# Kernel optimization log

Hardware: AMD Instinct MI355X
Metric: run time of the kernel (lower is better)

## Reference

```python
import jax, jax.numpy as jnp
import numpy as np
from jax import lax


def _farthest_point_sample(xyz, npoint):
    """Iterative FPS, faithful to the torch loop. xyz: [B,N,3] -> centroids [B,npoint] int32."""
    B, N, _ = xyz.shape
    barycenter = jnp.mean(xyz, axis=1, keepdims=True)            # [B,1,3]
    d0 = jnp.sum((xyz - barycenter) ** 2, axis=-1)               # [B,N]
    farthest = jnp.argmax(d0, axis=1)                            # [B]
    distance = jnp.full((B, N), 1e10, dtype=xyz.dtype)
    selected = jnp.zeros((B, N), dtype=bool)
    batch_idx = jnp.arange(B)

    def step(carry, _):
        distance, selected, farthest = carry
        selected = selected.at[batch_idx, farthest].set(True)
        centroid = jnp.take_along_axis(xyz, farthest[:, None, None], axis=1)  # [B,1,3]
        d = jnp.sum((xyz - centroid) ** 2, axis=-1)              # [B,N]
        d = jnp.where(selected, 0.0, d)                          # torch: dist[selected_mask]=0
        distance = jnp.minimum(distance, d)                      # torch: distance[mask]=dist[mask]
        nxt = jnp.argmax(distance, axis=-1)
        return (distance, selected, nxt), farthest

    _, cents = lax.scan(step, (distance, selected, farthest), None, length=npoint)
    return jnp.transpose(cents)                                   # [B, npoint]


def _assign_points_to_clusters(xyz, centroids):
    """Assign every point to nearest centroid. Vectorized over batch (no python loop)."""
    cpts = jnp.take_along_axis(xyz, centroids[:, :, None], axis=1)          # [B,P,3]
    # [B,N,P] pairwise squared distances
    dist = jnp.sum((xyz[:, :, None, :] - cpts[:, None, :, :]) ** 2, axis=-1)
    return jnp.argmin(dist, axis=-1)                                         # [B,N]


def setup_inputs() -> dict:
    key = jax.random.key(0)
    B, N = 8, 100000
    xyz = jax.random.normal(key, (B, N, 3), dtype=jnp.float32)
    return {"xyz": xyz, "npoint": 64}


def reference(xyz, npoint):
    centroids = _farthest_point_sample(xyz, npoint)               # [B,P] int
    clusters = _assign_points_to_clusters(xyz, centroids)         # [B,N] int
    centroid_xyz = jnp.take_along_axis(xyz, centroids[:, :, None], axis=1)  # [B,P,3] float
    return centroid_xyz, centroids, clusters
```

## Files before the change

### kernel.cpp

```cpp
#include <hip/hip_runtime.h>

#define BATCHES 8
#define NPTS    100000
#define NPOINT  64
#define BPB     16
#define NTHREADS 512
#define WPB     (NTHREADS / 64)
#define TPB     (BPB * NTHREADS)
#define KMAX    13
#define TAILN   (NPTS - (KMAX - 1) * TPB)

#define WS_BARY_OFF 0
#define WS_CNT_OFF  3072
#define WS_SLOT_OFF 4096
#define WS_CTRL_BYTES (WS_SLOT_OFF + BATCHES * NPOINT * BPB * 8)

__device__ __forceinline__ float sq3(float dx, float dy, float dz) {
    return __fadd_rn(__fadd_rn(__fmul_rn(dx, dx), __fmul_rn(dy, dy)), __fmul_rn(dz, dz));
}

__global__ __launch_bounds__(NTHREADS, 4)
void fps_kernel(const float* __restrict__ xyz, float* __restrict__ out,
                unsigned char* __restrict__ ws)
{
    double* baryPart = (double*)(ws + WS_BARY_OFF);
    unsigned int* cnt = (unsigned int*)(ws + WS_CNT_OFF);
    unsigned long long* slots = (unsigned long long*)(ws + WS_SLOT_OFF);

    const int b    = blockIdx.x & 7;
    const int blk  = blockIdx.x >> 3;
    const int tid  = threadIdx.x;
    const int wid  = tid >> 6;
    const int lane = tid & 63;
    const int t    = blk * NTHREADS + tid;

    const float* xb = xyz + (size_t)b * NPTS * 3;

    __shared__ double bred[WPB][3];
    __shared__ unsigned long long kred[WPB];
    __shared__ float s_c[3];
    __shared__ int s_far;

    float px[KMAX], py[KMAX], pz[KMAX], dist[KMAX];
    float bestd[KMAX]; int besti[KMAX];
    const int nk = (t < TAILN) ? KMAX : (KMAX - 1);

    double sx = 0.0, sy = 0.0, sz = 0.0;
    #pragma unroll
    for (int k = 0; k < KMAX; k++) {
        if (k < nk) {
            int p = t + k * TPB;
            float x = xb[p * 3 + 0], y = xb[p * 3 + 1], z = xb[p * 3 + 2];
            px[k] = x; py[k] = y; pz[k] = z; dist[k] = 1e10f;
            bestd[k] = 3.4e38f; besti[k] = 0;
            sx += (double)x; sy += (double)y; sz += (double)z;
        }
    }
    for (int off = 32; off > 0; off >>= 1) {
        sx += __shfl_down(sx, off); sy += __shfl_down(sy, off); sz += __shfl_down(sz, off);
    }
    if (lane == 0) { bred[wid][0] = sx; bred[wid][1] = sy; bred[wid][2] = sz; }
    __syncthreads();
    if (tid == 0) {
        double ax = 0, ay = 0, az = 0;
        for (int w = 0; w < WPB; w++) { ax += bred[w][0]; ay += bred[w][1]; az += bred[w][2]; }
        double* dst = baryPart + ((size_t)b * BPB + blk) * 3;
        dst[0] = ax; dst[1] = ay; dst[2] = az;
        __hip_atomic_fetch_add(&cnt[b], 1u, __ATOMIC_ACQ_REL, __HIP_MEMORY_SCOPE_AGENT);
        while (__hip_atomic_load(&cnt[b], __ATOMIC_ACQUIRE, __HIP_MEMORY_SCOPE_AGENT) < BPB)
            __builtin_amdgcn_s_sleep(2);
        double mx = 0, my = 0, mz = 0;
        for (int q = 0; q < BPB; q++) {
            const double* s2 = baryPart + ((size_t)b * BPB + q) * 3;
            mx += s2[0]; my += s2[1]; mz += s2[2];
        }
        s_c[0] = (float)(mx / (double)NPTS);
        s_c[1] = (float)(my / (double)NPTS);
        s_c[2] = (float)(mz / (double)NPTS);
    }
    __syncthreads();
    const float bx = s_c[0], by = s_c[1], bz = s_c[2];

    float bd = -1.0f; int bp = 0;
    #pragma unroll
    for (int k = 0; k < KMAX; k++) {
        if (k < nk) {
            int p = t + k * TPB;
            float d = sq3(__fsub_rn(px[k], bx), __fsub_rn(py[k], by), __fsub_rn(pz[k], bz));
            if (d > bd) { bd = d; bp = p; }
        }
    }
    unsigned long long key = (((unsigned long long)__float_as_uint(bd)) << 32)
                             | (unsigned)(0xFFFFFFFFu - (unsigned)bp);

    for (int e = 0; e < NPOINT; e++) {
        unsigned long long wmax = key;
        for (int m = 32; m > 0; m >>= 1) {
            unsigned long long o = __shfl_xor(wmax, m); if (o > wmax) wmax = o;
        }
        if (lane == 0) kred[wid] = wmax;
        __syncthreads();

        if (wid == 0) {
            unsigned long long v = (lane < WPB) ? kred[lane] : 0ull;
            for (int m = 4; m > 0; m >>= 1) {
                unsigned long long o = __shfl_xor(v, m, 8); if (o > v) v = o;
            }
            unsigned long long* row = &slots[((size_t)b * NPOINT + e) * BPB];
            if (lane == 0)
                __hip_atomic_store(&row[blk], v, __ATOMIC_RELAXED, __HIP_MEMORY_SCOPE_AGENT);
            unsigned long long w = 0;
            if (lane < BPB) {
                while ((w = __hip_atomic_load(&row[lane], __ATOMIC_RELAXED,
                                              __HIP_MEMORY_SCOPE_AGENT)) == 0ull) { }
            }
            for (int m = 8; m > 0; m >>= 1) {
                unsigned long long o = __shfl_xor(w, m, 16); if (o > w) w = o;
            }
            if (lane == 0) {
                int f = (int)(0xFFFFFFFFu - (unsigned)(w & 0xFFFFFFFFull));
                float cx = xb[f * 3 + 0], cy = xb[f * 3 + 1], cz = xb[f * 3 + 2];
                s_far = f; s_c[0] = cx; s_c[1] = cy; s_c[2] = cz;
                if (blk == 0) {
                    out[((size_t)b * NPOINT + e) * 3 + 0] = cx;
                    out[((size_t)b * NPOINT + e) * 3 + 1] = cy;
                    out[((size_t)b * NPOINT + e) * 3 + 2] = cz;
                    out[(size_t)BATCHES * NPOINT * 3 + b * NPOINT + e] = (float)f;
                }
            }
        }
        __syncthreads();
        if (e == NPOINT - 1) break;

        const float cx = s_c[0], cy = s_c[1], cz = s_c[2];
        bd = -1.0f; bp = 0;
        #pragma unroll
        for (int k = 0; k < KMAX; k++) {
            if (k < nk) {
                float d = sq3(__fsub_rn(px[k], cx), __fsub_rn(py[k], cy), __fsub_rn(pz[k], cz));
                if (d < bestd[k]) { bestd[k] = d; besti[k] = e; }
                float nd = fminf(dist[k], d);
                dist[k] = nd;
                int p = t + k * TPB;
                if (nd > bd) { bd = nd; bp = p; }
            }
        }
        key = (((unsigned long long)__float_as_uint(bd)) << 32)
              | (unsigned)(0xFFFFFFFFu - (unsigned)bp);
    }

    {
        const float cx = s_c[0], cy = s_c[1], cz = s_c[2];
        #pragma unroll
        for (int k = 0; k < KMAX; k++) {
            if (k < nk) {
                float d = sq3(__fsub_rn(px[k], cx), __fsub_rn(py[k], cy), __fsub_rn(pz[k], cz));
                if (d < bestd[k]) { bestd[k] = d; besti[k] = NPOINT - 1; }
            }
        }
    }

    float* outClust = out + (size_t)BATCHES * NPOINT * 3 + (size_t)BATCHES * NPOINT;
    #pragma unroll
    for (int k = 0; k < KMAX; k++)
        if (k < nk) outClust[(size_t)b * NPTS + t + k * TPB] = (float)besti[k];
}

extern "C" void kernel_launch(void* const* d_in, const int* in_sizes, int n_in,
                              void* d_out, int out_size, void* d_ws, size_t ws_size,
                              hipStream_t stream) {
    const float* xyz = (const float*)d_in[0];
    float* out = (float*)d_out;
    hipMemsetAsync(d_ws, 0, WS_CTRL_BYTES, stream);
    fps_kernel<<<dim3(BATCHES * BPB), dim3(NTHREADS), 0, stream>>>(
        xyz, out, (unsigned char*)d_ws);
}
```

Measured before the change: 149.2 us.

## Carry winning centroid coords through tagged slots, shrink workspace memset

Each block now publishes the winning point's coordinates alongside its key, writing four tagged 64-bit words per block. Consumers can then read the centroid directly instead of making a dependent global load of xyz after the cross-block reduction. Per-iteration tags replace zero-initialization, so the large slot-region memset shrinks to just the control area. Slots are padded by SU to spread them across cache lines. The cost is more atomic traffic per step, and the design depends on stale workspace never accidentally matching a tag, plus possible out-of-range writes if the workspace is smaller than the SU=4 layout needs.

New measurement: 239.9 us. 60.8% more time.

```diff
diff --git a/kernel.cpp b/kernel.cpp
--- a/kernel.cpp
+++ b/kernel.cpp
@@ -13,7 +13,7 @@
 #define WS_BARY_OFF 0
 #define WS_CNT_OFF  3072
 #define WS_SLOT_OFF 4096
-#define WS_CTRL_BYTES (WS_SLOT_OFF + BATCHES * NPOINT * BPB * 8)
+#define WS_ZERO_BYTES 4096
 
 __device__ __forceinline__ float sq3(float dx, float dy, float dz) {
     return __fadd_rn(__fadd_rn(__fmul_rn(dx, dx), __fmul_rn(dy, dy)), __fmul_rn(dz, dz));
@@ -21,7 +21,7 @@
 
 __global__ __launch_bounds__(NTHREADS, 4)
 void fps_kernel(const float* __restrict__ xyz, float* __restrict__ out,
-                unsigned char* __restrict__ ws)
+                unsigned char* __restrict__ ws, int SU )
 {
     double* baryPart = (double*)(ws + WS_BARY_OFF);
     unsigned int* cnt = (unsigned int*)(ws + WS_CNT_OFF);
@@ -37,9 +37,8 @@
     const float* xb = xyz + (size_t)b * NPTS * 3;
 
     __shared__ double bred[WPB][3];
-    __shared__ unsigned long long kred[WPB];
+    __shared__ unsigned long long kcomb[WPB][5];
     __shared__ float s_c[3];
-    __shared__ int s_far;
 
     float px[KMAX], py[KMAX], pz[KMAX], dist[KMAX];
     float bestd[KMAX]; int besti[KMAX];
@@ -81,13 +80,13 @@
     __syncthreads();
     const float bx = s_c[0], by = s_c[1], bz = s_c[2];
 
-    float bd = -1.0f; int bp = 0;
+    float bd = -1.0f, bpx = 0.f, bpy = 0.f, bpz = 0.f; int bp = 0;
     #pragma unroll
     for (int k = 0; k < KMAX; k++) {
         if (k < nk) {
             int p = t + k * TPB;
             float d = sq3(__fsub_rn(px[k], bx), __fsub_rn(py[k], by), __fsub_rn(pz[k], bz));
-            if (d > bd) { bd = d; bp = p; }
+            if (d > bd) { bd = d; bp = p; bpx = px[k]; bpy = py[k]; bpz = pz[k]; }
         }
     }
     unsigned long long key = (((unsigned long long)__float_as_uint(bd)) << 32)
@@ -98,29 +97,56 @@
         for (int m = 32; m > 0; m >>= 1) {
             unsigned long long o = __shfl_xor(wmax, m); if (o > wmax) wmax = o;
         }
-        if (lane == 0) kred[wid] = wmax;
+        if (key == wmax) {
+            kcomb[wid][0] = wmax;
+            kcomb[wid][1] = (((unsigned long long)__float_as_uint(bpx)) << 32)
+                            | (0x5A5A0000u | ((unsigned)e << 8) | 1u);
+            kcomb[wid][2] = (((unsigned long long)__float_as_uint(bpy)) << 32)
+                            | (0x5A5A0000u | ((unsigned)e << 8) | 2u);
+            kcomb[wid][3] = (((unsigned long long)__float_as_uint(bpz)) << 32)
+                            | (0x5A5A0000u | ((unsigned)e << 8) | 3u);
+        }
         __syncthreads();
 
         if (wid == 0) {
-            unsigned long long v = (lane < WPB) ? kred[lane] : 0ull;
+            unsigned long long* srow = slots + ((size_t)b * NPOINT + e) * BPB * SU;
+            unsigned long long v = (lane < WPB) ? kcomb[lane][0] : 0ull;
+            unsigned long long bb = v;
             for (int m = 4; m > 0; m >>= 1) {
-                unsigned long long o = __shfl_xor(v, m, 8); if (o > v) v = o;
-            }
-            unsigned long long* row = &slots[((size_t)b * NPOINT + e) * BPB];
-            if (lane == 0)
-                __hip_atomic_store(&row[blk], v, __ATOMIC_RELAXED, __HIP_MEMORY_SCOPE_AGENT);
-            unsigned long long w = 0;
-            if (lane < BPB) {
-                while ((w = __hip_atomic_load(&row[lane], __ATOMIC_RELAXED,
-                                              __HIP_MEMORY_SCOPE_AGENT)) == 0ull) { }
-            }
-            for (int m = 8; m > 0; m >>= 1) {
-                unsigned long long o = __shfl_xor(w, m, 16); if (o > w) w = o;
-            }
+                unsigned long long o = __shfl_xor(bb, m, 8); if (o > bb) bb = o;
+            }
+            unsigned long long bmask = __ballot(v == bb && lane < WPB);
+            int winwid = __ffsll(bmask) - 1;
+            if (lane < 4) {
+                unsigned long long wv = kcomb[winwid][lane];
+                __hip_atomic_store(&srow[(size_t)blk * SU + lane], wv,
+                                   __ATOMIC_RELAXED, __HIP_MEMORY_SCOPE_AGENT);
+            }
+            const int sl = lane >> 2, j = lane & 3;
+            unsigned long long* myp = &srow[(size_t)sl * SU + j];
+            const unsigned ctag = 0x5A5A0000u | ((unsigned)e << 8) | (unsigned)j;
+            unsigned long long val;
+            for (;;) {
+                val = __hip_atomic_load(myp, __ATOMIC_RELAXED, __HIP_MEMORY_SCOPE_AGENT);
+                unsigned lo = (unsigned)val;
+                bool ok = (j == 0) ? (lo >= 0xFFFE0000u) : (lo == ctag);
+                if (ok) break;
+            }
+            unsigned long long kv = (j == 0) ? val : 0ull;
+            for (int m = 32; m > 0; m >>= 1) {
+                unsigned long long o = __shfl_xor(kv, m); if (o > kv) kv = o;
+            }
+            unsigned long long mask = __ballot(val == kv);
+            int src = __ffsll(mask) - 1;
+            unsigned long long xw = __shfl(val, src + 1);
+            unsigned long long yw = __shfl(val, src + 2);
+            unsigned long long zw = __shfl(val, src + 3);
             if (lane == 0) {
-                int f = (int)(0xFFFFFFFFu - (unsigned)(w & 0xFFFFFFFFull));
-                float cx = xb[f * 3 + 0], cy = xb[f * 3 + 1], cz = xb[f * 3 + 2];
-                s_far = f; s_c[0] = cx; s_c[1] = cy; s_c[2] = cz;
+                int f = (int)(0xFFFFFFFFu - (unsigned)(kv & 0xFFFFFFFFull));
+                float cx = __uint_as_float((unsigned)(xw >> 32));
+                float cy = __uint_as_float((unsigned)(yw >> 32));
+                float cz = __uint_as_float((unsigned)(zw >> 32));
+                s_c[0] = cx; s_c[1] = cy; s_c[2] = cz;
                 if (blk == 0) {
                     out[((size_t)b * NPOINT + e) * 3 + 0] = cx;
                     out[((size_t)b * NPOINT + e) * 3 + 1] = cy;
@@ -133,7 +159,7 @@
         if (e == NPOINT - 1) break;
 
         const float cx = s_c[0], cy = s_c[1], cz = s_c[2];
-        bd = -1.0f; bp = 0;
+        bd = -1.0f; bp = 0; bpx = 0.f; bpy = 0.f; bpz = 0.f;
         #pragma unroll
         for (int k = 0; k < KMAX; k++) {
             if (k < nk) {
@@ -142,7 +168,7 @@
                 float nd = fminf(dist[k], d);
                 dist[k] = nd;
                 int p = t + k * TPB;
-                if (nd > bd) { bd = nd; bp = p; }
+                if (nd > bd) { bd = nd; bp = p; bpx = px[k]; bpy = py[k]; bpz = pz[k]; }
             }
         }
         key = (((unsigned long long)__float_as_uint(bd)) << 32)
@@ -171,7 +197,11 @@
                               hipStream_t stream) {
     const float* xyz = (const float*)d_in[0];
     float* out = (float*)d_out;
-    hipMemsetAsync(d_ws, 0, WS_CTRL_BYTES, stream);
+    int SU = 16;
+    if (ws_size < WS_SLOT_OFF + (size_t)BATCHES * NPOINT * BPB * 16 * 8) SU = 4;
+    if (ws_size < WS_SLOT_OFF + (size_t)BATCHES * NPOINT * BPB * 4 * 8)  SU = 1;
+    if (SU < 4) SU = 4;
+    hipMemsetAsync(d_ws, 0, WS_ZERO_BYTES, stream);
     fps_kernel<<<dim3(BATCHES * BPB), dim3(NTHREADS), 0, stream>>>(
-        xyz, out, (unsigned char*)d_ws);
+        xyz, out, (unsigned char*)d_ws, SU);
 }
```
